# Optimization experiments

Measured on AMD Instinct MI355X. Metric: run time of the kernel, lower is better.

The kernel has to match this reference:

```python
import jax, jax.numpy as jnp
import numpy as np

DELTA_COEFF = 1.0
CLAMP_MIN = 1e-3  # hardcoded in original clamp(min=0.001)


def setup_inputs() -> dict:
    key = jax.random.key(0)
    k1, k2, k3 = jax.random.split(key, 3)
    B, N, F_in, F_out = 2, 1024, 128, 64
    x = jax.random.normal(k1, (B, N, F_in), dtype=jnp.float32)
    adj = jax.random.uniform(k2, (B, N, N), dtype=jnp.float32)
    weight = jax.random.normal(k3, (F_in, F_out), dtype=jnp.float32) * (1.0 / np.sqrt(F_in))
    bias = jnp.zeros((F_out,), dtype=jnp.float32)
    return {"x": x, "adj": adj, "weight": weight, "bias": bias}


def reference(x, adj, weight, bias):
    # x: [B,N,F_in], adj: [B,N,N]
    x = x @ weight  # [B,N,F_out]
    B, N, _ = adj.shape
    # pairwise L1 distance: [B,N,N]
    abs_diff = jnp.sum(jnp.abs(x[:, :, None, :] - x[:, None, :, :]), axis=-1)
    mod_adj = adj / jnp.maximum(abs_diff, CLAMP_MIN)
    deg = jnp.sum(mod_adj, axis=-1)  # [B,N]
    # Laplacian L = D - A~ ; then I - delta * L
    lap = jnp.zeros_like(mod_adj).at[:, jnp.arange(N), jnp.arange(N)].set(deg) - mod_adj
    mod = jnp.eye(N, dtype=x.dtype) - DELTA_COEFF * lap
    out = jnp.matmul(mod, x) + bias
    return out
```

## Files before the change

kernel.cpp:

```cpp
#include <hip/hip_runtime.h>


#define JS 16

__device__ __forceinline__ void fma4(float4& a, float s, const float4 v) {
    a.x += s * v.x; a.y += s * v.y; a.z += s * v.z; a.w += s * v.w;
}

__global__ __launch_bounds__(256) void gemm_xw(const float* __restrict__ x,
                                               const float* __restrict__ w,
                                               float* __restrict__ xw) {
    __shared__ float ws_[128 * 64];
    __shared__ float xs[16 * 132];
    const int tid = threadIdx.x;
    const int r0  = blockIdx.x * 16;

#pragma unroll
    for (int e = tid; e < 2048; e += 256)
        ((float4*)ws_)[e] = ((const float4*)w)[e];
#pragma unroll
    for (int e = tid; e < 512; e += 256) {
        int row = e >> 5, c = e & 31;
        float4 v = *(const float4*)&x[(size_t)(r0 + row) * 128 + c * 4];
        *(float4*)&xs[row * 132 + c * 4] = v;
    }
    __syncthreads();

    const int rl = tid >> 4;
    const int fg = tid & 15;
    float4 acc = {0.f, 0.f, 0.f, 0.f};
#pragma unroll 8
    for (int k = 0; k < 128; ++k) {
        float xv = xs[rl * 132 + k];
        float4 wv = *(const float4*)&ws_[k * 64 + 4 * fg];
        fma4(acc, xv, wv);
    }
    *(float4*)&xw[(size_t)(r0 + rl) * 64 + 4 * fg] = acc;
}

template <bool ATOMIC>
__global__ __launch_bounds__(256) void fused_gtv(const float* __restrict__ xw,
                                                 const float* __restrict__ adj,
                                                 float* __restrict__ pout,
                                                 float* __restrict__ pdeg) {
    __shared__ float xi[64 * 64];
    __shared__ float xj[64 * 64];
    __shared__ float wt[64 * 68];

    const int tid = threadIdx.x;
    const int bx  = blockIdx.x;
    const int js  = bx & 15;
    const int it  = (bx >> 4) & 15;
    const int b   = bx >> 8;
    const int i0  = it * 64;
    const int j0  = js * 64;

    const float* xwb  = xw  + (size_t)b * 65536;
    const float* adjb = adj + (size_t)b * 1048576;

    const int ty = tid >> 4;
    const int tx = tid & 15;

    float4 av[4];
#pragma unroll
    for (int r = 0; r < 4; ++r)
        av[r] = *(const float4*)&adjb[(size_t)(i0 + 4 * ty + r) * 1024 + j0 + 4 * tx];

#pragma unroll
    for (int e = tid; e < 1024; e += 256) {
        int row = e >> 4, c = e & 15;
        int sc  = (c ^ ((row >> 2) & 7)) << 2;
        float4 vi = *(const float4*)&xwb[(i0 + row) * 64 + c * 4];
        float4 vj = *(const float4*)&xwb[(j0 + row) * 64 + c * 4];
        *(float4*)&xi[row * 64 + sc] = vi;
        *(float4*)&xj[row * 64 + sc] = vj;
    }
    __syncthreads();

    float d[4][4];
#pragma unroll
    for (int r = 0; r < 4; ++r)
#pragma unroll
        for (int q = 0; q < 4; ++q) d[r][q] = 0.f;

    const int sy = ty & 7, sx = tx & 7;
#pragma unroll
    for (int c = 0; c < 16; ++c) {
        float4 a[4], bb[4];
#pragma unroll
        for (int r = 0; r < 4; ++r)
            a[r] = *(const float4*)&xi[(4 * ty + r) * 64 + ((c ^ sy) << 2)];
#pragma unroll
        for (int q = 0; q < 4; ++q)
            bb[q] = *(const float4*)&xj[(4 * tx + q) * 64 + ((c ^ sx) << 2)];
#pragma unroll
        for (int r = 0; r < 4; ++r)
#pragma unroll
            for (int q = 0; q < 4; ++q) {
                float t0 = a[r].x - bb[q].x;
                float t1 = a[r].y - bb[q].y;
                float t2 = a[r].z - bb[q].z;
                float t3 = a[r].w - bb[q].w;
                d[r][q] += (fabsf(t0) + fabsf(t1)) + (fabsf(t2) + fabsf(t3));
            }
    }

    {
        const float* ac[4] = {&av[0].x, &av[1].x, &av[2].x, &av[3].x};
#pragma unroll
        for (int r = 0; r < 4; ++r)
#pragma unroll
            for (int q = 0; q < 4; ++q)
                wt[(4 * tx + q) * 68 + 4 * ty + r] = ac[r][q] / fmaxf(d[r][q], 1e-3f);
    }
    __syncthreads();

    const int i4 = tid >> 4;
    const int fg = tid & 15;
    float4 acc[4] = {{0,0,0,0},{0,0,0,0},{0,0,0,0},{0,0,0,0}};
    float  dg[4]  = {0.f, 0.f, 0.f, 0.f};
#pragma unroll 4
    for (int j = 0; j < 64; ++j) {
        float4 wv = *(const float4*)&wt[j * 68 + 4 * i4];
        float4 xv = *(const float4*)&xj[j * 64 + ((fg ^ ((j >> 2) & 7)) << 2)];
        fma4(acc[0], wv.x, xv);
        fma4(acc[1], wv.y, xv);
        fma4(acc[2], wv.z, xv);
        fma4(acc[3], wv.w, xv);
        dg[0] += wv.x; dg[1] += wv.y; dg[2] += wv.z; dg[3] += wv.w;
    }

    if (ATOMIC) {
#pragma unroll
        for (int r = 0; r < 4; ++r) {
            float* op = pout + ((size_t)b * 1024 + i0 + 4 * i4 + r) * 64 + 4 * fg;
            atomicAdd(&op[0], acc[r].x);
            atomicAdd(&op[1], acc[r].y);
            atomicAdd(&op[2], acc[r].z);
            atomicAdd(&op[3], acc[r].w);
            if (fg == 0) atomicAdd(&pdeg[b * 1024 + i0 + 4 * i4 + r], dg[r]);
        }
    } else {
        const size_t slot = (size_t)(js * 2 + b) * 65536;
#pragma unroll
        for (int r = 0; r < 4; ++r) {
            *(float4*)&pout[slot + (i0 + 4 * i4 + r) * 64 + 4 * fg] = acc[r];
            if (fg == 0) pdeg[(js * 2 + b) * 1024 + i0 + 4 * i4 + r] = dg[r];
        }
    }
}

template <bool ATOMIC>
__global__ __launch_bounds__(256) void finish_gtv(const float* __restrict__ xw,
                                                  const float* __restrict__ part,
                                                  const float* __restrict__ pdeg,
                                                  const float* __restrict__ bias,
                                                  float* __restrict__ out) {
    int idx = blockIdx.x * 256 + threadIdx.x;
    int f = idx & 63;
    int r = idx >> 6;
    int b = r >> 10;
    if (ATOMIC) {
        out[idx] = out[idx] + (1.f - pdeg[r]) * xw[idx] + bias[f];
    } else {
        int loc = idx & 65535;
        int n   = r & 1023;
        float s = 0.f, dgs = 0.f;
#pragma unroll
        for (int js = 0; js < JS; ++js) {
            s   += part[(size_t)(js * 2 + b) * 65536 + loc];
            dgs += pdeg[(js * 2 + b) * 1024 + n];
        }
        out[idx] = s + (1.f - dgs) * xw[idx] + bias[f];
    }
}

extern "C" void kernel_launch(void* const* d_in, const int* in_sizes, int n_in,
                              void* d_out, int out_size, void* d_ws, size_t ws_size,
                              hipStream_t stream) {
    const float* x    = (const float*)d_in[0];
    const float* adj  = (const float*)d_in[1];
    const float* w    = (const float*)d_in[2];
    const float* bias = (const float*)d_in[3];
    float* out = (float*)d_out;

    float* xw   = (float*)d_ws;
    float* pdeg = (float*)((char*)d_ws + 512 * 1024);
    float* part = (float*)((char*)d_ws + 512 * 1024 + 128 * 1024);
    const size_t NEED = 512 * 1024 + 128 * 1024 + (size_t)32 * 65536 * 4;

    gemm_xw<<<128, 256, 0, stream>>>(x, w, xw);

    if (ws_size >= NEED) {
        fused_gtv<false><<<512, 256, 0, stream>>>(xw, adj, part, pdeg);
        finish_gtv<false><<<512, 256, 0, stream>>>(xw, part, pdeg, bias, out);
    } else {
        hipMemsetAsync(out, 0, 2 * 1024 * 64 * sizeof(float), stream);
        hipMemsetAsync(pdeg, 0, 2 * 1024 * sizeof(float), stream);
        fused_gtv<true><<<512, 256, 0, stream>>>(xw, adj, out, pdeg);
        finish_gtv<true><<<512, 256, 0, stream>>>(xw, nullptr, pdeg, bias, out);
    }
}
```

Before: 91.20 us.

## Compute pairwise L1 distances in packed fp16 and halve the i-tile size

The GEMM now also writes an fp16 copy of x@W, and the fused kernel computes pairwise L1 distances with packed half2 sub/abs/add instead of fp32, halving shared-memory traffic and ALU ops for the distance step. The i-tile shrinks from 64 to 32 rows, doubling the grid to 1024 blocks, and the GEMM uses 8-row tiles for more blocks. Accumulating 16 terms per lane in fp16 loses precision in the distances, which feed a division and may breach tolerance, and the per-block aggregation work changes.

```diff
diff --git a/kernel.cpp b/kernel.cpp
--- a/kernel.cpp
+++ b/kernel.cpp
@@ -1,7 +1,9 @@
 #include <hip/hip_runtime.h>
+#include <hip/hip_fp16.h>
 
 
 #define JS 16
+#define HSTR 72
 
 __device__ __forceinline__ void fma4(float4& a, float s, const float4 v) {
     a.x += s * v.x; a.y += s * v.y; a.z += s * v.z; a.w += s * v.w;
@@ -9,143 +11,156 @@
 
 __global__ __launch_bounds__(256) void gemm_xw(const float* __restrict__ x,
                                                const float* __restrict__ w,
-                                               float* __restrict__ xw) {
+                                               float* __restrict__ xw,
+                                               __half* __restrict__ xwh) {
     __shared__ float ws_[128 * 64];
-    __shared__ float xs[16 * 132];
+    __shared__ float xs[8 * 132];
     const int tid = threadIdx.x;
-    const int r0  = blockIdx.x * 16;
+    const int r0  = blockIdx.x * 8;
 
 #pragma unroll
     for (int e = tid; e < 2048; e += 256)
         ((float4*)ws_)[e] = ((const float4*)w)[e];
-#pragma unroll
-    for (int e = tid; e < 512; e += 256) {
-        int row = e >> 5, c = e & 31;
+    {
+        int row = tid >> 5, c = tid & 31;
         float4 v = *(const float4*)&x[(size_t)(r0 + row) * 128 + c * 4];
         *(float4*)&xs[row * 132 + c * 4] = v;
     }
     __syncthreads();
 
-    const int rl = tid >> 4;
-    const int fg = tid & 15;
-    float4 acc = {0.f, 0.f, 0.f, 0.f};
+    const int rl = tid >> 5;
+    const int fg = tid & 31;
+    float2 acc = {0.f, 0.f};
 #pragma unroll 8
     for (int k = 0; k < 128; ++k) {
         float xv = xs[rl * 132 + k];
-        float4 wv = *(const float4*)&ws_[k * 64 + 4 * fg];
-        fma4(acc, xv, wv);
-    }
-    *(float4*)&xw[(size_t)(r0 + rl) * 64 + 4 * fg] = acc;
+        float2 wv = *(const float2*)&ws_[k * 64 + 2 * fg];
+        acc.x += xv * wv.x; acc.y += xv * wv.y;
+    }
+    size_t o = (size_t)(r0 + rl) * 64 + 2 * fg;
+    *(float2*)&xw[o] = acc;
+    *(__half2*)&xwh[o] = __floats2half2_rn(acc.x, acc.y);
 }
 
 template <bool ATOMIC>
 __global__ __launch_bounds__(256) void fused_gtv(const float* __restrict__ xw,
+                                                 const __half* __restrict__ xwh,
                                                  const float* __restrict__ adj,
                                                  float* __restrict__ pout,
                                                  float* __restrict__ pdeg) {
-    __shared__ float xi[64 * 64];
-    __shared__ float xj[64 * 64];
-    __shared__ float wt[64 * 68];
+    __shared__ __half xih[32 * HSTR];
+    __shared__ __half xjh[64 * HSTR];
+    __shared__ float  xjf[64 * 64];
+    __shared__ float  wt[64 * 36];
 
     const int tid = threadIdx.x;
     const int bx  = blockIdx.x;
     const int js  = bx & 15;
-    const int it  = (bx >> 4) & 15;
-    const int b   = bx >> 8;
-    const int i0  = it * 64;
+    const int it  = (bx >> 4) & 31;
+    const int b   = bx >> 9;
+    const int i0  = it * 32;
     const int j0  = js * 64;
 
-    const float* xwb  = xw  + (size_t)b * 65536;
-    const float* adjb = adj + (size_t)b * 1048576;
-
-    const int ty = tid >> 4;
-    const int tx = tid & 15;
-
-    float4 av[4];
+    const float*  xwb = xw  + (size_t)b * 65536;
+    const __half* xhb = xwh + (size_t)b * 65536;
+    const float*  adjb = adj + (size_t)b * 1048576;
+
+    const int ty = tid >> 5;
+    const int tx = tid & 31;
+
+    float2 av[4];
 #pragma unroll
     for (int r = 0; r < 4; ++r)
-        av[r] = *(const float4*)&adjb[(size_t)(i0 + 4 * ty + r) * 1024 + j0 + 4 * tx];
-
+        av[r] = *(const float2*)&adjb[(size_t)(i0 + 4 * ty + r) * 1024 + j0 + 2 * tx];
+
+    {
+        int row = tid >> 3, c = tid & 7;
+        float4 v = *(const float4*)&xhb[(i0 + row) * 64 + c * 8];
+        *(float4*)&xih[row * HSTR + c * 8] = v;
+    }
+#pragma unroll
+    for (int e = tid; e < 512; e += 256) {
+        int row = e >> 3, c = e & 7;
+        float4 v = *(const float4*)&xhb[(j0 + row) * 64 + c * 8];
+        *(float4*)&xjh[row * HSTR + c * 8] = v;
+    }
 #pragma unroll
     for (int e = tid; e < 1024; e += 256) {
         int row = e >> 4, c = e & 15;
-        int sc  = (c ^ ((row >> 2) & 7)) << 2;
-        float4 vi = *(const float4*)&xwb[(i0 + row) * 64 + c * 4];
-        float4 vj = *(const float4*)&xwb[(j0 + row) * 64 + c * 4];
-        *(float4*)&xi[row * 64 + sc] = vi;
-        *(float4*)&xj[row * 64 + sc] = vj;
+        float4 v = *(const float4*)&xwb[(j0 + row) * 64 + c * 4];
+        *(float4*)&xjf[row * 64 + c * 4] = v;
     }
     __syncthreads();
 
-    float d[4][4];
+    __half2 acc[4][2];
 #pragma unroll
     for (int r = 0; r < 4; ++r)
 #pragma unroll
-        for (int q = 0; q < 4; ++q) d[r][q] = 0.f;
-
-    const int sy = ty & 7, sx = tx & 7;
-#pragma unroll
-    for (int c = 0; c < 16; ++c) {
-        float4 a[4], bb[4];
+        for (int q = 0; q < 2; ++q) acc[r][q] = __floats2half2_rn(0.f, 0.f);
+
+#pragma unroll
+    for (int c = 0; c < 8; ++c) {
+        float4 a[4], bb[2];
 #pragma unroll
         for (int r = 0; r < 4; ++r)
-            a[r] = *(const float4*)&xi[(4 * ty + r) * 64 + ((c ^ sy) << 2)];
-#pragma unroll
-        for (int q = 0; q < 4; ++q)
-            bb[q] = *(const float4*)&xj[(4 * tx + q) * 64 + ((c ^ sx) << 2)];
-#pragma unroll
-        for (int r = 0; r < 4; ++r)
-#pragma unroll
-            for (int q = 0; q < 4; ++q) {
-                float t0 = a[r].x - bb[q].x;
-                float t1 = a[r].y - bb[q].y;
-                float t2 = a[r].z - bb[q].z;
-                float t3 = a[r].w - bb[q].w;
-                d[r][q] += (fabsf(t0) + fabsf(t1)) + (fabsf(t2) + fabsf(t3));
+            a[r] = *(const float4*)&xih[(4 * ty + r) * HSTR + c * 8];
+#pragma unroll
+        for (int q = 0; q < 2; ++q)
+            bb[q] = *(const float4*)&xjh[(2 * tx + q) * HSTR + c * 8];
+#pragma unroll
+        for (int r = 0; r < 4; ++r) {
+            const __half2* pa = (const __half2*)&a[r];
+#pragma unroll
+            for (int q = 0; q < 2; ++q) {
+                const __half2* pb = (const __half2*)&bb[q];
+#pragma unroll
+                for (int m = 0; m < 4; ++m)
+                    acc[r][q] = __hadd2(acc[r][q], __habs2(__hsub2(pa[m], pb[m])));
             }
-    }
-
-    {
-        const float* ac[4] = {&av[0].x, &av[1].x, &av[2].x, &av[3].x};
-#pragma unroll
-        for (int r = 0; r < 4; ++r)
-#pragma unroll
-            for (int q = 0; q < 4; ++q)
-                wt[(4 * tx + q) * 68 + 4 * ty + r] = ac[r][q] / fmaxf(d[r][q], 1e-3f);
+        }
+    }
+
+#pragma unroll
+    for (int q = 0; q < 2; ++q) {
+        float4 wq;
+        float* wp = &wq.x;
+#pragma unroll
+        for (int r = 0; r < 4; ++r) {
+            float d = __low2float(acc[r][q]) + __high2float(acc[r][q]);
+            wp[r] = (&av[r].x)[q] / fmaxf(d, 1e-3f);
+        }
+        *(float4*)&wt[(2 * tx + q) * 36 + 4 * ty] = wq;
     }
     __syncthreads();
 
-    const int i4 = tid >> 4;
+    const int i2 = tid >> 4;
     const int fg = tid & 15;
-    float4 acc[4] = {{0,0,0,0},{0,0,0,0},{0,0,0,0},{0,0,0,0}};
-    float  dg[4]  = {0.f, 0.f, 0.f, 0.f};
-#pragma unroll 4
+    float4 acc2[2] = {{0,0,0,0},{0,0,0,0}};
+    float  dg[2]   = {0.f, 0.f};
+#pragma unroll 8
     for (int j = 0; j < 64; ++j) {
-        float4 wv = *(const float4*)&wt[j * 68 + 4 * i4];
-        float4 xv = *(const float4*)&xj[j * 64 + ((fg ^ ((j >> 2) & 7)) << 2)];
-        fma4(acc[0], wv.x, xv);
-        fma4(acc[1], wv.y, xv);
-        fma4(acc[2], wv.z, xv);
-        fma4(acc[3], wv.w, xv);
-        dg[0] += wv.x; dg[1] += wv.y; dg[2] += wv.z; dg[3] += wv.w;
+        float2 wv = *(const float2*)&wt[j * 36 + 2 * i2];
+        float4 xv = *(const float4*)&xjf[j * 64 + 4 * fg];
+        fma4(acc2[0], wv.x, xv);
+        fma4(acc2[1], wv.y, xv);
+        dg[0] += wv.x; dg[1] += wv.y;
     }
 
     if (ATOMIC) {
 #pragma unroll
-        for (int r = 0; r < 4; ++r) {
-            float* op = pout + ((size_t)b * 1024 + i0 + 4 * i4 + r) * 64 + 4 * fg;
-            atomicAdd(&op[0], acc[r].x);
-            atomicAdd(&op[1], acc[r].y);
-            atomicAdd(&op[2], acc[r].z);
-            atomicAdd(&op[3], acc[r].w);
-            if (fg == 0) atomicAdd(&pdeg[b * 1024 + i0 + 4 * i4 + r], dg[r]);
+        for (int r = 0; r < 2; ++r) {
+            float* op = pout + ((size_t)b * 1024 + i0 + 2 * i2 + r) * 64 + 4 * fg;
+            float* ap = &acc2[r].x;
+#pragma unroll
+            for (int m = 0; m < 4; ++m) atomicAdd(&op[m], ap[m]);
+            if (fg == 0) atomicAdd(&pdeg[b * 1024 + i0 + 2 * i2 + r], dg[r]);
         }
     } else {
         const size_t slot = (size_t)(js * 2 + b) * 65536;
 #pragma unroll
-        for (int r = 0; r < 4; ++r) {
-            *(float4*)&pout[slot + (i0 + 4 * i4 + r) * 64 + 4 * fg] = acc[r];
-            if (fg == 0) pdeg[(js * 2 + b) * 1024 + i0 + 4 * i4 + r] = dg[r];
+        for (int r = 0; r < 2; ++r) {
+            *(float4*)&pout[slot + (i0 + 2 * i2 + r) * 64 + 4 * fg] = acc2[r];
+            if (fg == 0) pdeg[(js * 2 + b) * 1024 + i0 + 2 * i2 + r] = dg[r];
         }
     }
 }
@@ -184,20 +199,22 @@
     const float* bias = (const float*)d_in[3];
     float* out = (float*)d_out;
 
-    float* xw   = (float*)d_ws;
-    float* pdeg = (float*)((char*)d_ws + 512 * 1024);
-    float* part = (float*)((char*)d_ws + 512 * 1024 + 128 * 1024);
-    const size_t NEED = 512 * 1024 + 128 * 1024 + (size_t)32 * 65536 * 4;
-
-    gemm_xw<<<128, 256, 0, stream>>>(x, w, xw);
+    char* wsb = (char*)d_ws;
+    float*  xw   = (float*)wsb;
+    __half* xwh  = (__half*)(wsb + 512 * 1024);
+    float*  pdeg = (float*)(wsb + 768 * 1024);
+    float*  part = (float*)(wsb + 896 * 1024);
+    const size_t NEED = 896 * 1024 + (size_t)32 * 65536 * 4;
+
+    gemm_xw<<<256, 256, 0, stream>>>(x, w, xw, xwh);
 
     if (ws_size >= NEED) {
-        fused_gtv<false><<<512, 256, 0, stream>>>(xw, adj, part, pdeg);
+        fused_gtv<false><<<1024, 256, 0, stream>>>(xw, xwh, adj, part, pdeg);
         finish_gtv<false><<<512, 256, 0, stream>>>(xw, part, pdeg, bias, out);
     } else {
         hipMemsetAsync(out, 0, 2 * 1024 * 64 * sizeof(float), stream);
         hipMemsetAsync(pdeg, 0, 2 * 1024 * sizeof(float), stream);
-        fused_gtv<true><<<512, 256, 0, stream>>>(xw, adj, out, pdeg);
+        fused_gtv<true><<<1024, 256, 0, stream>>>(xw, xwh, adj, out, pdeg);
         finish_gtv<true><<<512, 256, 0, stream>>>(xw, nullptr, pdeg, bias, out);
     }
 }
```

After: 88.27 us. -3.2%, faster.
